# Performance work log

Measured on AMD Instinct MI355X. Metric: run time of the kernel, lower is better.

The kernel has to match this reference:

```python
import jax, jax.numpy as jnp
import numpy as np

ALPHA = 1.5
N_ITER = 50
B, N, C = 8, 1024, 1024
H = 8
D = C // H


def entmax_bisect(x, alpha=ALPHA, n_iter=N_ITER):
    # entmax-bisect (Peters et al. 2019), matching the entmax package's bisection.
    xm = (alpha - 1.0) * x
    d = xm.shape[-1]
    inv = 1.0 / (alpha - 1.0)  # = 2.0 for alpha=1.5
    max_val = jnp.max(xm, axis=-1, keepdims=True)
    tau_lo = max_val - 1.0                                   # gp(1, alpha) = 1
    tau_hi = max_val - (1.0 / d) ** (alpha - 1.0)            # gp(1/d, alpha)
    f_lo = jnp.sum(jnp.maximum(xm - tau_lo, 0.0) ** inv, axis=-1, keepdims=True) - 1.0
    dm0 = tau_hi - tau_lo

    def body(_, carry):
        tau_lo, dm, tau_m = carry
        dm = dm * 0.5
        tau_m = tau_lo + dm
        f_m = jnp.sum(jnp.maximum(xm - tau_m, 0.0) ** inv, axis=-1, keepdims=True) - 1.0
        tau_lo = jnp.where(f_m * f_lo >= 0, tau_m, tau_lo)
        return (tau_lo, dm, tau_m)

    _, _, tau_m = jax.lax.fori_loop(0, n_iter, body, (tau_lo, dm0, tau_lo))
    p = jnp.maximum(xm - tau_m, 0.0) ** inv
    return p / jnp.sum(p, axis=-1, keepdims=True)


def setup_inputs() -> dict:
    key = jax.random.key(0)
    ks = jax.random.split(key, 9)
    s = 0.02
    return {
        "x": jax.random.normal(ks[0], (B, N, C), dtype=jnp.float32),
        "Wq": jax.random.normal(ks[1], (C, C), dtype=jnp.float32) * s,
        "bq": jnp.zeros((C,), dtype=jnp.float32),
        "Wk": jax.random.normal(ks[2], (C, C), dtype=jnp.float32) * s,
        "bk": jnp.zeros((C,), dtype=jnp.float32),
        "Wv": jax.random.normal(ks[3], (C, C), dtype=jnp.float32) * s,
        "bv": jnp.zeros((C,), dtype=jnp.float32),
        "Wo": jax.random.normal(ks[4], (C, C), dtype=jnp.float32) * s,
        "bo": jnp.zeros((C,), dtype=jnp.float32),
    }


def reference(x, Wq, bq, Wk, bk, Wv, bv, Wo, bo):
    b, n, c = x.shape
    def proj(W, bias):
        return (x @ W + bias).reshape(b, n, H, D).transpose(0, 2, 1, 3)  # [B,H,N,D]
    q = proj(Wq, bq)
    k = proj(Wk, bk)
    v = proj(Wv, bv)
    scores = jnp.einsum("bhnd,bhmd->bhnm", q, k) / (D ** 0.5)  # [B,H,N,N]
    attn = entmax_bisect(scores)
    ctx = jnp.einsum("bhnm,bhmd->bhnd", attn, v)
    ctx = ctx.transpose(0, 2, 1, 3).reshape(b, n, c)
    out = ctx @ Wo + bo
    return (out, attn)
```

## Files before the change

### kernel.cpp

```cpp
#include <hip/hip_runtime.h>

#define DEV __device__ __forceinline__

typedef _Float16 f16;
typedef _Float16 f16x8 __attribute__((ext_vector_type(8)));
typedef float f32x4 __attribute__((ext_vector_type(4)));


DEV void gload_lds16(const f16* g, f16* l) {
  __builtin_amdgcn_global_load_lds(
      (const __attribute__((address_space(1))) void*)g,
      (__attribute__((address_space(3))) void*)l, 16, 0, 0);
}

DEV float wred_max(float v) {
#pragma unroll
  for (int o = 32; o > 0; o >>= 1) v = fmaxf(v, __shfl_xor(v, o, 64));
  return v;
}
DEV float wred_sum(float v) {
#pragma unroll
  for (int o = 32; o > 0; o >>= 1) v += __shfl_xor(v, o, 64);
  return v;
}


__global__ __launch_bounds__(256) void cast_f32_f16(const float* __restrict__ in,
                                                    f16* __restrict__ out, int n) {
  int i = (blockIdx.x * 256 + threadIdx.x) * 4;
  if (i < n) {
    float4 f = *(const float4*)(in + i);
    f16 o0 = (f16)f.x, o1 = (f16)f.y, o2 = (f16)f.z, o3 = (f16)f.w;
    f16* d = out + i;
    d[0] = o0; d[1] = o1; d[2] = o2; d[3] = o3;
  }
}

__global__ __launch_bounds__(256) void transpose_cast(
    const float* s0, const float* s1, const float* s2, const float* s3,
    f16* d0, f16* d1, f16* d2, f16* d3) {
  const float* S[4] = {s0, s1, s2, s3};
  f16* D[4] = {d0, d1, d2, d3};
  const float* W = S[blockIdx.z];
  f16* WT = D[blockIdx.z];
  __shared__ float tile[32][33];
  int tx = threadIdx.x, ty = threadIdx.y;
  int r0 = blockIdx.y * 32, c0 = blockIdx.x * 32;
#pragma unroll
  for (int i = 0; i < 32; i += 8) tile[ty + i][tx] = W[(r0 + ty + i) * 1024 + c0 + tx];
  __syncthreads();
#pragma unroll
  for (int i = 0; i < 32; i += 8) WT[(c0 + ty + i) * 1024 + r0 + tx] = (f16)tile[tx][ty + i];
}


DEV void gemm_bt_f16(const f16* __restrict__ A, const f16* __restrict__ B,
                     int lda, int ldb, int K, f16* As, f16* Bs, f32x4 (&acc)[4][4]) {
  const int t = threadIdx.x;
  const int l = t & 63, w = t >> 6;
  const int wm = w >> 1, wn = w & 1;
  const f16* ag = A + (t >> 2) * lda + (t & 3) * 8;
  const f16* bg = B + (t >> 2) * ldb + (t & 3) * 8;
  f16* asd = As + w * 512;
  f16* bsd = Bs + w * 512;
  const int arow = wm * 64 + (l & 15);
  const int brow = wn * 64 + (l & 15);
  const int ko = (l >> 4) * 8;
  for (int k0 = 0; k0 < K; k0 += 32) {
    __syncthreads();
    gload_lds16(ag + k0, asd);
    gload_lds16(ag + 64 * lda + k0, asd + 2048);
    gload_lds16(bg + k0, bsd);
    gload_lds16(bg + 64 * ldb + k0, bsd + 2048);
    __syncthreads();
    f16x8 af[4], bf[4];
#pragma unroll
    for (int i = 0; i < 4; i++) af[i] = *(const f16x8*)(As + (arow + i * 16) * 32 + ko);
#pragma unroll
    for (int j = 0; j < 4; j++) bf[j] = *(const f16x8*)(Bs + (brow + j * 16) * 32 + ko);
#pragma unroll
    for (int i = 0; i < 4; i++)
#pragma unroll
      for (int j = 0; j < 4; j++)
        acc[i][j] = __builtin_amdgcn_mfma_f32_16x16x32_f16(af[i], bf[j], acc[i][j], 0, 0, 0);
  }
}


__global__ __launch_bounds__(256) void qkv_gemm(
    const f16* __restrict__ xb, const f16* __restrict__ WTq, const f16* __restrict__ WTk,
    const f16* __restrict__ WTv, const float* __restrict__ bq, const float* __restrict__ bk,
    const float* __restrict__ bv, f16* __restrict__ q, f16* __restrict__ kk,
    f16* __restrict__ vT) {
  __shared__ f16 As[128 * 32];
  __shared__ f16 Bs[128 * 32];
  __shared__ f16 tr[128 * 132];
  const int z = blockIdx.z;
  const f16* WT = (z == 0) ? WTq : ((z == 1) ? WTk : WTv);
  const float* bias = (z == 0) ? bq : ((z == 1) ? bk : bv);
  const int rowBase = blockIdx.y * 128, colBase = blockIdx.x * 128;
  f32x4 zero4 = {0.f, 0.f, 0.f, 0.f};
  f32x4 acc[4][4];
#pragma unroll
  for (int i = 0; i < 4; i++)
#pragma unroll
    for (int j = 0; j < 4; j++) acc[i][j] = zero4;
  gemm_bt_f16(xb + rowBase * 1024, WT + colBase * 1024, 1024, 1024, 1024, As, Bs, acc);
  const int t = threadIdx.x, l = t & 63, w = t >> 6, wm = w >> 1, wn = w & 1;
  if (z < 2) {
    f16* dst = (z == 0) ? q : kk;
#pragma unroll
    for (int i = 0; i < 4; i++)
#pragma unroll
      for (int j = 0; j < 4; j++)
#pragma unroll
        for (int r = 0; r < 4; r++) {
          int rt = wm * 64 + i * 16 + ((l >> 4) << 2) + r;
          int ct = wn * 64 + j * 16 + (l & 15);
          int rr = rowBase + rt, c = colBase + ct;
          float val = acc[i][j][r] + bias[c];
          int b = rr >> 10, n = rr & 1023, h = c >> 7, d = c & 127;
          dst[((b * 8 + h) * 1024 + n) * 128 + d] = (f16)val;
        }
  } else {
#pragma unroll
    for (int i = 0; i < 4; i++)
#pragma unroll
      for (int j = 0; j < 4; j++)
#pragma unroll
        for (int r = 0; r < 4; r++) {
          int rt = wm * 64 + i * 16 + ((l >> 4) << 2) + r;
          int ct = wn * 64 + j * 16 + (l & 15);
          tr[ct * 132 + rt] = (f16)(acc[i][j][r] + bias[colBase + ct]);
        }
    __syncthreads();
    int b = blockIdx.y >> 3, h = blockIdx.x;
    int nb = (blockIdx.y & 7) * 128;
    int head = b * 8 + h;
#pragma unroll
    for (int p = 0; p < 8; p++) {
      int lin = p * 2048 + t * 8;
      int c = lin >> 7, r = lin & 127;
      const f16* src = &tr[c * 132 + r];
      uint2 a0 = *(const uint2*)(src);
      uint2 a1 = *(const uint2*)(src + 4);
      f16* dst = vT + head * 131072 + c * 1024 + nb + r;
      *(uint2*)(dst) = a0;
      *(uint2*)(dst + 4) = a1;
    }
  }
}


__global__ __launch_bounds__(256) void scores_gemm(const f16* __restrict__ q,
                                                   const f16* __restrict__ kk,
                                                   float* __restrict__ xm) {
  __shared__ f16 As[128 * 32];
  __shared__ f16 Bs[128 * 32];
  const int head = blockIdx.z;
  const int rowBase = blockIdx.y * 128, colBase = blockIdx.x * 128;
  f32x4 zero4 = {0.f, 0.f, 0.f, 0.f};
  f32x4 acc[4][4];
#pragma unroll
  for (int i = 0; i < 4; i++)
#pragma unroll
    for (int j = 0; j < 4; j++) acc[i][j] = zero4;
  gemm_bt_f16(q + head * 131072 + rowBase * 128, kk + head * 131072 + colBase * 128,
              128, 128, 128, As, Bs, acc);
  const float SC = 0.04419417382415922f;
  const int l = threadIdx.x & 63, w = threadIdx.x >> 6, wm = w >> 1, wn = w & 1;
  float* out = xm + (size_t)head * 1048576;
#pragma unroll
  for (int i = 0; i < 4; i++)
#pragma unroll
    for (int j = 0; j < 4; j++)
#pragma unroll
      for (int r = 0; r < 4; r++) {
        int rt = wm * 64 + i * 16 + ((l >> 4) << 2) + r;
        int ct = wn * 64 + j * 16 + (l & 15);
        out[(size_t)(rowBase + rt) * 1024 + colBase + ct] = acc[i][j][r] * SC;
      }
}


__global__ __launch_bounds__(512) void entmax_rows(float* __restrict__ attn) {
  const int l = threadIdx.x & 63, w = threadIdx.x >> 6;
  float* x = attn + ((size_t)blockIdx.x * 8 + w) * 1024;
  float xr[16];
#pragma unroll
  for (int j = 0; j < 4; j++) {
    float4 v = *(const float4*)(x + j * 256 + l * 4);
    xr[4 * j + 0] = v.x; xr[4 * j + 1] = v.y; xr[4 * j + 2] = v.z; xr[4 * j + 3] = v.w;
  }
  float mx = xr[0];
#pragma unroll
  for (int e = 1; e < 16; e++) mx = fmaxf(mx, xr[e]);
  mx = wred_max(mx);
  float tau_lo = mx - 1.0f;
  float tau_hi = mx - 0.03125f;
  float dm = tau_hi - tau_lo;
  float s = 0.f;
#pragma unroll
  for (int e = 0; e < 16; e++) { float tv = fmaxf(xr[e] - tau_lo, 0.f); s = fmaf(tv, tv, s); }
  s = wred_sum(s);
  const float f_lo = s - 1.0f;
  float tau_m = tau_lo;
  for (int it = 0; it < 32; ++it) {
    dm *= 0.5f;
    tau_m = tau_lo + dm;
    float sm = 0.f;
#pragma unroll
    for (int e = 0; e < 16; e++) { float tv = fmaxf(xr[e] - tau_m, 0.f); sm = fmaf(tv, tv, sm); }
    sm = wred_sum(sm);
    if ((sm - 1.0f) * f_lo >= 0.f) tau_lo = tau_m;
  }
  float p[16];
  float ps = 0.f;
#pragma unroll
  for (int e = 0; e < 16; e++) { float tv = fmaxf(xr[e] - tau_m, 0.f); p[e] = tv * tv; ps += p[e]; }
  ps = wred_sum(ps);
  float inv = 1.0f / ps;
#pragma unroll
  for (int j = 0; j < 4; j++) {
    float4 v;
    v.x = p[4 * j + 0] * inv; v.y = p[4 * j + 1] * inv;
    v.z = p[4 * j + 2] * inv; v.w = p[4 * j + 3] * inv;
    *(float4*)(x + j * 256 + l * 4) = v;
  }
}


__global__ __launch_bounds__(256) void ctx_gemm(const float* __restrict__ attn,
                                                const f16* __restrict__ vT,
                                                f16* __restrict__ ctx) {
  __shared__ f16 As[128 * 32];
  __shared__ f16 Bs[128 * 32];
  const int head = blockIdx.z;
  const int rowBase = blockIdx.y * 128;
  const int t = threadIdx.x, l = t & 63, w = t >> 6, wm = w >> 1, wn = w & 1;
  f32x4 zero4 = {0.f, 0.f, 0.f, 0.f};
  f32x4 acc[4][4];
#pragma unroll
  for (int i = 0; i < 4; i++)
#pragma unroll
    for (int j = 0; j < 4; j++) acc[i][j] = zero4;
  const float* Ag = attn + (size_t)head * 1048576 + (size_t)(rowBase + (t >> 1)) * 1024 + (t & 1) * 16;
  const f16* bg = vT + head * 131072 + (t >> 2) * 1024 + (t & 3) * 8;
  f16* bsd = Bs + w * 512;
  f16* asw = As + (t >> 1) * 32 + (t & 1) * 16;
  const int arow = wm * 64 + (l & 15), brow = wn * 64 + (l & 15), ko = (l >> 4) * 8;
  for (int k0 = 0; k0 < 1024; k0 += 32) {
    __syncthreads();
    gload_lds16(bg + k0, bsd);
    gload_lds16(bg + 64 * 1024 + k0, bsd + 2048);
    float4 f0 = *(const float4*)(Ag + k0);
    float4 f1 = *(const float4*)(Ag + k0 + 4);
    float4 f2 = *(const float4*)(Ag + k0 + 8);
    float4 f3 = *(const float4*)(Ag + k0 + 12);
    f16x8 h0 = {(f16)f0.x, (f16)f0.y, (f16)f0.z, (f16)f0.w,
                (f16)f1.x, (f16)f1.y, (f16)f1.z, (f16)f1.w};
    f16x8 h1 = {(f16)f2.x, (f16)f2.y, (f16)f2.z, (f16)f2.w,
                (f16)f3.x, (f16)f3.y, (f16)f3.z, (f16)f3.w};
    *(f16x8*)asw = h0;
    *(f16x8*)(asw + 8) = h1;
    __syncthreads();
    f16x8 af[4], bf[4];
#pragma unroll
    for (int i = 0; i < 4; i++) af[i] = *(const f16x8*)(As + (arow + i * 16) * 32 + ko);
#pragma unroll
    for (int j = 0; j < 4; j++) bf[j] = *(const f16x8*)(Bs + (brow + j * 16) * 32 + ko);
#pragma unroll
    for (int i = 0; i < 4; i++)
#pragma unroll
      for (int j = 0; j < 4; j++)
        acc[i][j] = __builtin_amdgcn_mfma_f32_16x16x32_f16(af[i], bf[j], acc[i][j], 0, 0, 0);
  }
  int b = head >> 3, h = head & 7;
#pragma unroll
  for (int i = 0; i < 4; i++)
#pragma unroll
    for (int j = 0; j < 4; j++)
#pragma unroll
      for (int r = 0; r < 4; r++) {
        int rt = wm * 64 + i * 16 + ((l >> 4) << 2) + r;
        int ct = wn * 64 + j * 16 + (l & 15);
        int n = rowBase + rt;
        ctx[(size_t)(b * 1024 + n) * 1024 + h * 128 + ct] = (f16)acc[i][j][r];
      }
}


__global__ __launch_bounds__(256) void out_gemm(const f16* __restrict__ ctx,
                                                const f16* __restrict__ WTo,
                                                const float* __restrict__ bo,
                                                float* __restrict__ out) {
  __shared__ f16 As[128 * 32];
  __shared__ f16 Bs[128 * 32];
  const int rowBase = blockIdx.y * 128, colBase = blockIdx.x * 128;
  f32x4 zero4 = {0.f, 0.f, 0.f, 0.f};
  f32x4 acc[4][4];
#pragma unroll
  for (int i = 0; i < 4; i++)
#pragma unroll
    for (int j = 0; j < 4; j++) acc[i][j] = zero4;
  gemm_bt_f16(ctx + rowBase * 1024, WTo + colBase * 1024, 1024, 1024, 1024, As, Bs, acc);
  const int l = threadIdx.x & 63, w = threadIdx.x >> 6, wm = w >> 1, wn = w & 1;
#pragma unroll
  for (int i = 0; i < 4; i++)
#pragma unroll
    for (int j = 0; j < 4; j++)
#pragma unroll
      for (int r = 0; r < 4; r++) {
        int rt = wm * 64 + i * 16 + ((l >> 4) << 2) + r;
        int ct = wn * 64 + j * 16 + (l & 15);
        out[(size_t)(rowBase + rt) * 1024 + colBase + ct] = acc[i][j][r] + bo[colBase + ct];
      }
}


extern "C" void kernel_launch(void* const* d_in, const int* in_sizes, int n_in,
                              void* d_out, int out_size, void* d_ws, size_t ws_size,
                              hipStream_t stream) {
  const float* x  = (const float*)d_in[0];
  const float* Wq = (const float*)d_in[1];
  const float* bq = (const float*)d_in[2];
  const float* Wk = (const float*)d_in[3];
  const float* bk = (const float*)d_in[4];
  const float* Wv = (const float*)d_in[5];
  const float* bv = (const float*)d_in[6];
  const float* Wo = (const float*)d_in[7];
  const float* bo = (const float*)d_in[8];
  float* out = (float*)d_out;
  float* attn = out + 8388608;

  char* ws = (char*)d_ws;
  f16* xb  = (f16*)(ws);
  f16* ctx = (f16*)(ws);
  f16* WTq = (f16*)(ws + (16u << 20));
  f16* WTk = (f16*)(ws + (18u << 20));
  f16* WTv = (f16*)(ws + (20u << 20));
  f16* WTo = (f16*)(ws + (22u << 20));
  f16* q   = (f16*)(ws + (24u << 20));
  f16* kk  = (f16*)(ws + (40u << 20));
  f16* vT  = (f16*)(ws + (56u << 20));

  cast_f32_f16<<<dim3(8192), dim3(256), 0, stream>>>(x, xb, 8388608);
  transpose_cast<<<dim3(32, 32, 4), dim3(32, 8), 0, stream>>>(
      Wq, Wk, Wv, Wo, WTq, WTk, WTv, WTo);
  qkv_gemm<<<dim3(8, 64, 3), dim3(256), 0, stream>>>(
      xb, WTq, WTk, WTv, bq, bk, bv, q, kk, vT);
  scores_gemm<<<dim3(8, 8, 64), dim3(256), 0, stream>>>(q, kk, attn);
  entmax_rows<<<dim3(8192), dim3(512), 0, stream>>>(attn);
  ctx_gemm<<<dim3(1, 8, 64), dim3(256), 0, stream>>>(attn, vT, ctx);
  out_gemm<<<dim3(8, 64), dim3(256), 0, stream>>>(ctx, WTo, bo, out);
}
```

Measured before the change: 696.7 us.

## Store scores and probabilities as fp16 scratch, halve bisection iterations

The scores GEMM now writes fp16 scores to a separate workspace buffer, and the entmax kernel reads them from there. It writes the fp32 attention output and also an fp16 copy of the probabilities in place. The context GEMM then consumes the fp16 probabilities through the shared gemm_bt_f16 path instead of reloading and converting fp32 rows. This cuts HBM traffic on the large B*H*N*N intermediate. The bisection loop also drops from 32 to 16 iterations, which reduces the precision of tau and the fp16 scores reduce input precision, so accuracy against the reference may suffer.

```diff
diff --git a/kernel.cpp b/kernel.cpp
--- a/kernel.cpp
+++ b/kernel.cpp
@@ -154,7 +154,7 @@
 
 __global__ __launch_bounds__(256) void scores_gemm(const f16* __restrict__ q,
                                                    const f16* __restrict__ kk,
-                                                   float* __restrict__ xm) {
+                                                   f16* __restrict__ xm16) {
   __shared__ f16 As[128 * 32];
   __shared__ f16 Bs[128 * 32];
   const int head = blockIdx.z;
@@ -169,7 +169,7 @@
               128, 128, 128, As, Bs, acc);
   const float SC = 0.04419417382415922f;
   const int l = threadIdx.x & 63, w = threadIdx.x >> 6, wm = w >> 1, wn = w & 1;
-  float* out = xm + (size_t)head * 1048576;
+  f16* out = xm16 + (size_t)head * 1048576;
 #pragma unroll
   for (int i = 0; i < 4; i++)
 #pragma unroll
@@ -178,20 +178,22 @@
       for (int r = 0; r < 4; r++) {
         int rt = wm * 64 + i * 16 + ((l >> 4) << 2) + r;
         int ct = wn * 64 + j * 16 + (l & 15);
-        out[(size_t)(rowBase + rt) * 1024 + colBase + ct] = acc[i][j][r] * SC;
+        out[(size_t)(rowBase + rt) * 1024 + colBase + ct] = (f16)(acc[i][j][r] * SC);
       }
 }
 
 
-__global__ __launch_bounds__(512) void entmax_rows(float* __restrict__ attn) {
+__global__ __launch_bounds__(512) void entmax_rows(f16* __restrict__ xm16,
+                                                   float* __restrict__ attn) {
   const int l = threadIdx.x & 63, w = threadIdx.x >> 6;
-  float* x = attn + ((size_t)blockIdx.x * 8 + w) * 1024;
+  const size_t row = (size_t)blockIdx.x * 8 + w;
+  f16* xp = xm16 + row * 1024;
+  float* ap = attn + row * 1024;
+  f16x8 h0 = *(const f16x8*)(xp + l * 8);
+  f16x8 h1 = *(const f16x8*)(xp + 512 + l * 8);
   float xr[16];
 #pragma unroll
-  for (int j = 0; j < 4; j++) {
-    float4 v = *(const float4*)(x + j * 256 + l * 4);
-    xr[4 * j + 0] = v.x; xr[4 * j + 1] = v.y; xr[4 * j + 2] = v.z; xr[4 * j + 3] = v.w;
-  }
+  for (int e = 0; e < 8; e++) { xr[e] = (float)h0[e]; xr[8 + e] = (float)h1[e]; }
   float mx = xr[0];
 #pragma unroll
   for (int e = 1; e < 16; e++) mx = fmaxf(mx, xr[e]);
@@ -205,7 +207,7 @@
   s = wred_sum(s);
   const float f_lo = s - 1.0f;
   float tau_m = tau_lo;
-  for (int it = 0; it < 32; ++it) {
+  for (int it = 0; it < 16; ++it) {
     dm *= 0.5f;
     tau_m = tau_lo + dm;
     float sm = 0.f;
@@ -220,61 +222,39 @@
   for (int e = 0; e < 16; e++) { float tv = fmaxf(xr[e] - tau_m, 0.f); p[e] = tv * tv; ps += p[e]; }
   ps = wred_sum(ps);
   float inv = 1.0f / ps;
-#pragma unroll
-  for (int j = 0; j < 4; j++) {
-    float4 v;
-    v.x = p[4 * j + 0] * inv; v.y = p[4 * j + 1] * inv;
-    v.z = p[4 * j + 2] * inv; v.w = p[4 * j + 3] * inv;
-    *(float4*)(x + j * 256 + l * 4) = v;
-  }
-}
-
-
-__global__ __launch_bounds__(256) void ctx_gemm(const float* __restrict__ attn,
+  float4 v0 = {p[0] * inv, p[1] * inv, p[2] * inv, p[3] * inv};
+  float4 v1 = {p[4] * inv, p[5] * inv, p[6] * inv, p[7] * inv};
+  float4 v2 = {p[8] * inv, p[9] * inv, p[10] * inv, p[11] * inv};
+  float4 v3 = {p[12] * inv, p[13] * inv, p[14] * inv, p[15] * inv};
+  *(float4*)(ap + l * 8) = v0;
+  *(float4*)(ap + l * 8 + 4) = v1;
+  *(float4*)(ap + 512 + l * 8) = v2;
+  *(float4*)(ap + 512 + l * 8 + 4) = v3;
+  f16x8 o0 = {(f16)v0.x, (f16)v0.y, (f16)v0.z, (f16)v0.w,
+              (f16)v1.x, (f16)v1.y, (f16)v1.z, (f16)v1.w};
+  f16x8 o1 = {(f16)v2.x, (f16)v2.y, (f16)v2.z, (f16)v2.w,
+              (f16)v3.x, (f16)v3.y, (f16)v3.z, (f16)v3.w};
+  *(f16x8*)(xp + l * 8) = o0;
+  *(f16x8*)(xp + 512 + l * 8) = o1;
+}
+
+
+__global__ __launch_bounds__(256) void ctx_gemm(const f16* __restrict__ p16,
                                                 const f16* __restrict__ vT,
                                                 f16* __restrict__ ctx) {
   __shared__ f16 As[128 * 32];
   __shared__ f16 Bs[128 * 32];
   const int head = blockIdx.z;
   const int rowBase = blockIdx.y * 128;
-  const int t = threadIdx.x, l = t & 63, w = t >> 6, wm = w >> 1, wn = w & 1;
   f32x4 zero4 = {0.f, 0.f, 0.f, 0.f};
   f32x4 acc[4][4];
 #pragma unroll
   for (int i = 0; i < 4; i++)
 #pragma unroll
     for (int j = 0; j < 4; j++) acc[i][j] = zero4;
-  const float* Ag = attn + (size_t)head * 1048576 + (size_t)(rowBase + (t >> 1)) * 1024 + (t & 1) * 16;
-  const f16* bg = vT + head * 131072 + (t >> 2) * 1024 + (t & 3) * 8;
-  f16* bsd = Bs + w * 512;
-  f16* asw = As + (t >> 1) * 32 + (t & 1) * 16;
-  const int arow = wm * 64 + (l & 15), brow = wn * 64 + (l & 15), ko = (l >> 4) * 8;
-  for (int k0 = 0; k0 < 1024; k0 += 32) {
-    __syncthreads();
-    gload_lds16(bg + k0, bsd);
-    gload_lds16(bg + 64 * 1024 + k0, bsd + 2048);
-    float4 f0 = *(const float4*)(Ag + k0);
-    float4 f1 = *(const float4*)(Ag + k0 + 4);
-    float4 f2 = *(const float4*)(Ag + k0 + 8);
-    float4 f3 = *(const float4*)(Ag + k0 + 12);
-    f16x8 h0 = {(f16)f0.x, (f16)f0.y, (f16)f0.z, (f16)f0.w,
-                (f16)f1.x, (f16)f1.y, (f16)f1.z, (f16)f1.w};
-    f16x8 h1 = {(f16)f2.x, (f16)f2.y, (f16)f2.z, (f16)f2.w,
-                (f16)f3.x, (f16)f3.y, (f16)f3.z, (f16)f3.w};
-    *(f16x8*)asw = h0;
-    *(f16x8*)(asw + 8) = h1;
-    __syncthreads();
-    f16x8 af[4], bf[4];
-#pragma unroll
-    for (int i = 0; i < 4; i++) af[i] = *(const f16x8*)(As + (arow + i * 16) * 32 + ko);
-#pragma unroll
-    for (int j = 0; j < 4; j++) bf[j] = *(const f16x8*)(Bs + (brow + j * 16) * 32 + ko);
-#pragma unroll
-    for (int i = 0; i < 4; i++)
-#pragma unroll
-      for (int j = 0; j < 4; j++)
-        acc[i][j] = __builtin_amdgcn_mfma_f32_16x16x32_f16(af[i], bf[j], acc[i][j], 0, 0, 0);
-  }
+  gemm_bt_f16(p16 + (size_t)head * 1048576 + (size_t)rowBase * 1024,
+              vT + head * 131072, 1024, 1024, 1024, As, Bs, acc);
+  const int l = threadIdx.x & 63, w = threadIdx.x >> 6, wm = w >> 1, wn = w & 1;
   int b = head >> 3, h = head & 7;
 #pragma unroll
   for (int i = 0; i < 4; i++)
@@ -343,14 +323,15 @@
   f16* q   = (f16*)(ws + (24u << 20));
   f16* kk  = (f16*)(ws + (40u << 20));
   f16* vT  = (f16*)(ws + (56u << 20));
+  f16* xm16= (f16*)(ws + (72u << 20));
 
   cast_f32_f16<<<dim3(8192), dim3(256), 0, stream>>>(x, xb, 8388608);
   transpose_cast<<<dim3(32, 32, 4), dim3(32, 8), 0, stream>>>(
       Wq, Wk, Wv, Wo, WTq, WTk, WTv, WTo);
   qkv_gemm<<<dim3(8, 64, 3), dim3(256), 0, stream>>>(
       xb, WTq, WTk, WTv, bq, bk, bv, q, kk, vT);
-  scores_gemm<<<dim3(8, 8, 64), dim3(256), 0, stream>>>(q, kk, attn);
-  entmax_rows<<<dim3(8192), dim3(512), 0, stream>>>(attn);
-  ctx_gemm<<<dim3(1, 8, 64), dim3(256), 0, stream>>>(attn, vT, ctx);
+  scores_gemm<<<dim3(8, 8, 64), dim3(256), 0, stream>>>(q, kk, xm16);
+  entmax_rows<<<dim3(8192), dim3(512), 0, stream>>>(xm16, attn);
+  ctx_gemm<<<dim3(1, 8, 64), dim3(256), 0, stream>>>(xm16, vT, ctx);
   out_gemm<<<dim3(8, 64), dim3(256), 0, stream>>>(ctx, WTo, bo, out);
 }
```

New measurement: 604.6 us. 13.2% less time.
